# Kernel optimization log

Measured on AMD Instinct MI355X. Metric: run time of the kernel, lower is better.

## Reference

```python
import jax, jax.numpy as jnp
import numpy as np

MODEL_DIM = 1024
H = 16
DK = MODEL_DIM // H


def setup_inputs() -> dict:
    key = jax.random.key(0)
    ks = jax.random.split(key, 11)
    B, S, D = 4, 2048, MODEL_DIM
    s = 1.0 / np.sqrt(D)
    inp = {
        "q": jax.random.normal(ks[0], (B, S, D), jnp.float32),
        "k": jax.random.normal(ks[1], (B, S, D), jnp.float32),
        "v": jax.random.normal(ks[2], (B, S, D), jnp.float32),
        # stacked per-head projection weights [H, D, DK] and biases [H, DK]
        "wq_w": jax.random.normal(ks[3], (H, D, DK), jnp.float32) * s,
        "wq_b": jax.random.normal(ks[4], (H, DK), jnp.float32) * s,
        "wk_w": jax.random.normal(ks[5], (H, D, DK), jnp.float32) * s,
        "wk_b": jax.random.normal(ks[6], (H, DK), jnp.float32) * s,
        "wv_w": jax.random.normal(ks[7], (H, D, DK), jnp.float32) * s,
        "wv_b": jax.random.normal(ks[8], (H, DK), jnp.float32) * s,
        "wo_w": jax.random.normal(ks[9], (D, D), jnp.float32) * s,
        "wo_b": jax.random.normal(ks[10], (D,), jnp.float32) * s,
    }
    return inp


def reference(q, k, v, wq_w, wq_b, wk_w, wk_b, wv_w, wv_b, wo_w, wo_b):
    # per-head projections, batched over heads: [B,S,D] x [H,D,DK] -> [B,H,S,DK]
    qh = jnp.einsum('bsd,hdk->bhsk', q, wq_w) + wq_b[None, :, None, :]
    kh = jnp.einsum('bsd,hdk->bhsk', k, wk_w) + wk_b[None, :, None, :]
    vh = jnp.einsum('bsd,hdk->bhsk', v, wv_w) + wv_b[None, :, None, :]
    scale = 1.0 / jnp.sqrt(jnp.asarray(DK, qh.dtype))
    scores = jnp.einsum('bhqk,bhsk->bhqs', qh, kh) * scale  # [B,H,S,S]
    out = jnp.einsum('bhqs,bhsk->bhqk', scores, vh)         # [B,H,S,DK]
    # NON-STANDARD: softmax applied AFTER the value matmul, over last dim (dv)
    out = jax.nn.softmax(out, axis=-1)
    # concat heads along feature dim: [B,S,H*DK]
    B, Hh, S, Dk = out.shape
    heads = jnp.transpose(out, (0, 2, 1, 3)).reshape(B, S, Hh * Dk)
    return heads @ wo_w.T + wo_b
```

## Files before the change

kernel.cpp:

```cpp
#include <hip/hip_runtime.h>
#include <math.h>

#define B 4
#define S 2048
#define D 1024
#define H 16
#define DK 64
#define MS (B * S)
#define GKA 2048

typedef short bf16x8 __attribute__((ext_vector_type(8)));
typedef float f32x4 __attribute__((ext_vector_type(4)));

__device__ __forceinline__ unsigned short f2bf(float x) {
  union { float f; unsigned u; } v; v.f = x;
  unsigned r = v.u + 0x7fff + ((v.u >> 16) & 1);
  return (unsigned short)(r >> 16);
}
__device__ __forceinline__ float bf2f(unsigned short h) {
  union { unsigned u; float f; } v; v.u = ((unsigned)h) << 16;
  return v.f;
}
__device__ __forceinline__ void split2(float x, unsigned short& hi, unsigned short& lo) {
  hi = f2bf(x);
  lo = f2bf(x - bf2f(hi));
}

__global__ __launch_bounds__(256) void split_a_kernel(
    const float* __restrict__ X0, const float* __restrict__ X1,
    unsigned short* __restrict__ O0, unsigned short* __restrict__ O1) {
  const float* X = blockIdx.z ? X1 : X0;
  unsigned short* O = blockIdx.z ? O1 : O0;
  int t = blockIdx.x * 256 + threadIdx.x;
  int idx = t * 4;
  int m = idx >> 10, d = idx & 1023;
  float4 x = *(const float4*)&X[idx];
  union { unsigned short h[4]; ushort4 u; } uh, ul;
  split2(x.x, uh.h[0], ul.h[0]);
  split2(x.y, uh.h[1], ul.h[1]);
  split2(x.z, uh.h[2], ul.h[2]);
  split2(x.w, uh.h[3], ul.h[3]);
  *(ushort4*)&O[(size_t)m * GKA + d] = uh.u;
  *(ushort4*)&O[(size_t)m * GKA + 1024 + d] = ul.u;
}

__global__ __launch_bounds__(256) void split_wp_kernel(
    const float* __restrict__ W0, const float* __restrict__ W1, const float* __restrict__ W2,
    unsigned short* __restrict__ O0, unsigned short* __restrict__ O1,
    unsigned short* __restrict__ O2) {
  const float* W = blockIdx.z == 0 ? W0 : (blockIdx.z == 1 ? W1 : W2);
  unsigned short* O = blockIdx.z == 0 ? O0 : (blockIdx.z == 1 ? O1 : O2);
  int t = blockIdx.x * 256 + threadIdx.x;
  int d = t & 1023, n = t >> 10;
  int h = n >> 6, dk = n & 63;
  float x = W[((size_t)(h << 10) + d) * 64 + dk];
  unsigned short hi, lo;
  split2(x, hi, lo);
  size_t ro = (size_t)n * GKA + d;
  O[ro] = hi;
  O[ro + 1024] = lo;
}

__global__ __launch_bounds__(256) void wo_cast_kernel(const float* __restrict__ W,
                                                      unsigned short* __restrict__ O) {
  int t = blockIdx.x * 256 + threadIdx.x;
  int idx = t * 4;
  float4 x = *(const float4*)&W[idx];
  ushort4 u;
  u.x = f2bf(x.x); u.y = f2bf(x.y); u.z = f2bf(x.z); u.w = f2bf(x.w);
  *(ushort4*)&O[idx] = u;
}

#define BK 32
template <int SPLIT>
__global__ __launch_bounds__(256) void gemm_kernel(
    const unsigned short* __restrict__ A0, const unsigned short* __restrict__ A1,
    const unsigned short* __restrict__ B0, const unsigned short* __restrict__ B1,
    const float* __restrict__ bias0, const float* __restrict__ bias1,
    float* __restrict__ C0, float* __restrict__ C1) {
  const int KLOG = SPLIT ? 3072 : 1024;
  const int AST = SPLIT ? 2048 : 1024;
  const int BST = SPLIT ? 2048 : 1024;
  const unsigned short* A = blockIdx.z ? A1 : A0;
  const unsigned short* BT = blockIdx.z ? B1 : B0;
  const float* bias = blockIdx.z ? bias1 : bias0;
  float* C = blockIdx.z ? C1 : C0;

  __shared__ __align__(16) unsigned short As[128 * BK];
  __shared__ __align__(16) unsigned short Bs[128 * BK];
  const int tid = threadIdx.x;
  const int lane = tid & 63;
  const int w = tid >> 6;
  const int wm = (w >> 1) * 64;
  const int wn = (w & 1) * 64;
  const size_t bm = (size_t)blockIdx.y * 128;
  const size_t bn = (size_t)blockIdx.x * 128;

  f32x4 acc[4][4];
#pragma unroll
  for (int i = 0; i < 4; i++)
#pragma unroll
    for (int j = 0; j < 4; j++) acc[i][j] = (f32x4){0.f, 0.f, 0.f, 0.f};

  const int srow = lane >> 2;
  const int skof = (lane & 3) * 8;
  const unsigned short* Ag0 = A + (bm + w * 32 + srow) * AST + skof;
  const unsigned short* Ag1 = Ag0 + (size_t)16 * AST;
  const unsigned short* Bg0 = BT + (bn + w * 32 + srow) * BST + skof;
  const unsigned short* Bg1 = Bg0 + (size_t)16 * BST;
  unsigned short* As0 = As + (w * 2) * 512;
  unsigned short* As1 = As0 + 512;
  unsigned short* Bs0 = Bs + (w * 2) * 512;
  unsigned short* Bs1 = Bs0 + 512;

  const int fm = lane & 15;
  const int fk = (lane >> 4) * 8;

  for (int k0 = 0; k0 < KLOG; k0 += BK) {
    const int aofs = SPLIT ? (k0 < 2048 ? k0 : k0 - 2048) : k0;
    const int bofs = SPLIT ? (k0 < 1024 ? k0 : k0 - 1024) : k0;
    __syncthreads();
    __builtin_amdgcn_global_load_lds((const __attribute__((address_space(1))) void*)(Ag0 + aofs),
                                     (__attribute__((address_space(3))) void*)As0, 16, 0, 0);
    __builtin_amdgcn_global_load_lds((const __attribute__((address_space(1))) void*)(Ag1 + aofs),
                                     (__attribute__((address_space(3))) void*)As1, 16, 0, 0);
    __builtin_amdgcn_global_load_lds((const __attribute__((address_space(1))) void*)(Bg0 + bofs),
                                     (__attribute__((address_space(3))) void*)Bs0, 16, 0, 0);
    __builtin_amdgcn_global_load_lds((const __attribute__((address_space(1))) void*)(Bg1 + bofs),
                                     (__attribute__((address_space(3))) void*)Bs1, 16, 0, 0);
    __syncthreads();
    bf16x8 af[4], bf[4];
#pragma unroll
    for (int i = 0; i < 4; i++) {
      af[i] = *(const bf16x8*)&As[(wm + i * 16 + fm) * BK + fk];
      bf[i] = *(const bf16x8*)&Bs[(wn + i * 16 + fm) * BK + fk];
    }
#pragma unroll
    for (int i = 0; i < 4; i++)
#pragma unroll
      for (int j = 0; j < 4; j++)
        acc[i][j] = __builtin_amdgcn_mfma_f32_16x16x32_bf16(af[i], bf[j], acc[i][j], 0, 0, 0);
  }

  const int r0 = (lane >> 4) * 4;
#pragma unroll
  for (int i = 0; i < 4; i++)
#pragma unroll
    for (int j = 0; j < 4; j++) {
      size_t row = bm + wm + i * 16 + r0;
      size_t col = bn + wn + j * 16 + fm;
      float bb = bias[col];
#pragma unroll
      for (int r = 0; r < 4; r++) C[(row + r) * D + col] = acc[i][j][r] + bb;
    }
}

__global__ __launch_bounds__(256) void compute_m_kernel(
    const float* __restrict__ KH, const float* __restrict__ VH, float* __restrict__ Mout) {
  const int sc = blockIdx.x, h = blockIdx.y, b = blockIdx.z;
  const int tid = threadIdx.x;
  const int i0 = (tid >> 4) * 4;
  const int j0 = (tid & 15) * 4;
  __shared__ float ks[16][64], vs[16][64];
  float acc[4][4];
#pragma unroll
  for (int a = 0; a < 4; a++)
#pragma unroll
    for (int c = 0; c < 4; c++) acc[a][c] = 0.f;

  const int s0 = sc * (S / 8);
  const int rr = tid >> 4;
  const int cc = (tid & 15) * 4;
  for (int s = s0; s < s0 + S / 8; s += 16) {
    size_t base = ((size_t)b * S + s + rr) * D + h * 64 + cc;
    __syncthreads();
    *(float4*)&ks[rr][cc] = *(const float4*)&KH[base];
    *(float4*)&vs[rr][cc] = *(const float4*)&VH[base];
    __syncthreads();
#pragma unroll
    for (int ss = 0; ss < 16; ss++) {
      float4 kf = *(const float4*)&ks[ss][i0];
      float4 vf = *(const float4*)&vs[ss][j0];
      float ka[4] = {kf.x, kf.y, kf.z, kf.w};
      float va[4] = {vf.x, vf.y, vf.z, vf.w};
#pragma unroll
      for (int a = 0; a < 4; a++)
#pragma unroll
        for (int c = 0; c < 4; c++) acc[a][c] += ka[a] * va[c];
    }
  }
  float* Mp = Mout + ((size_t)(b * H + h)) * DK * DK;
#pragma unroll
  for (int a = 0; a < 4; a++)
#pragma unroll
    for (int c = 0; c < 4; c++) atomicAdd(&Mp[(i0 + a) * DK + j0 + c], acc[a][c]);
}

__global__ __launch_bounds__(256) void split_m_kernel(const float* __restrict__ M,
                                                      unsigned short* __restrict__ MSP) {
  const int bh = blockIdx.x;
  const float* Mp = M + (size_t)bh * 4096;
  unsigned short* hiP = MSP + (size_t)bh * 8192;
  unsigned short* loP = hiP + 4096;
  for (int idx = threadIdx.x; idx < 4096; idx += 256) {
    int kk = idx >> 6, nn = idx & 63;
    unsigned short hi, lo;
    split2(Mp[idx], hi, lo);
    hiP[nn * 64 + kk] = hi;
    loP[nn * 64 + kk] = lo;
  }
}

__global__ __launch_bounds__(256) void qm_mfma_softmax_kernel(
    const float* __restrict__ QH, const unsigned short* __restrict__ MSP,
    unsigned short* __restrict__ HB) {
  const int sc = blockIdx.x, h = blockIdx.y, b = blockIdx.z;
  const int tid = threadIdx.x;
  const int lane = tid & 63;
  const int w = tid >> 6;

  const int fm = lane & 15;
  const int quad = lane >> 4;
  const int ko = quad * 8;

  const size_t rbase = (size_t)b * S + sc * 64 + w * 16;
  const float* qrow = QH + (rbase + fm) * D + h * 64;
  float qf[16];
  *(float4*)&qf[0] = *(const float4*)&qrow[ko];
  *(float4*)&qf[4] = *(const float4*)&qrow[ko + 4];
  *(float4*)&qf[8] = *(const float4*)&qrow[32 + ko];
  *(float4*)&qf[12] = *(const float4*)&qrow[32 + ko + 4];
  bf16x8 ahi0, alo0, ahi1, alo1;
#pragma unroll
  for (int j = 0; j < 8; j++) {
    unsigned short hi, lo;
    split2(qf[j], hi, lo);
    ahi0[j] = (short)hi; alo0[j] = (short)lo;
    split2(qf[8 + j], hi, lo);
    ahi1[j] = (short)hi; alo1[j] = (short)lo;
  }

  const unsigned short* hiP = MSP + ((size_t)(b * H + h)) * 8192;
  const unsigned short* loP = hiP + 4096;
  bf16x8 bhi[2][4], blo[2][4];
#pragma unroll
  for (int t = 0; t < 2; t++)
#pragma unroll
    for (int j = 0; j < 4; j++) {
      bhi[t][j] = *(const bf16x8*)&hiP[(j * 16 + fm) * 64 + t * 32 + ko];
      blo[t][j] = *(const bf16x8*)&loP[(j * 16 + fm) * 64 + t * 32 + ko];
    }

  f32x4 acc[4];
#pragma unroll
  for (int j = 0; j < 4; j++) acc[j] = (f32x4){0.f, 0.f, 0.f, 0.f};
#pragma unroll
  for (int j = 0; j < 4; j++) {
    acc[j] = __builtin_amdgcn_mfma_f32_16x16x32_bf16(ahi0, bhi[0][j], acc[j], 0, 0, 0);
    acc[j] = __builtin_amdgcn_mfma_f32_16x16x32_bf16(ahi1, bhi[1][j], acc[j], 0, 0, 0);
    acc[j] = __builtin_amdgcn_mfma_f32_16x16x32_bf16(alo0, bhi[0][j], acc[j], 0, 0, 0);
    acc[j] = __builtin_amdgcn_mfma_f32_16x16x32_bf16(alo1, bhi[1][j], acc[j], 0, 0, 0);
    acc[j] = __builtin_amdgcn_mfma_f32_16x16x32_bf16(ahi0, blo[0][j], acc[j], 0, 0, 0);
    acc[j] = __builtin_amdgcn_mfma_f32_16x16x32_bf16(ahi1, blo[1][j], acc[j], 0, 0, 0);
  }

  f32x4 l[4];
#pragma unroll
  for (int j = 0; j < 4; j++)
#pragma unroll
    for (int r = 0; r < 4; r++) l[j][r] = acc[j][r] * 0.125f;

  f32x4 mx = l[0];
#pragma unroll
  for (int j = 1; j < 4; j++)
#pragma unroll
    for (int r = 0; r < 4; r++) mx[r] = fmaxf(mx[r], l[j][r]);
#pragma unroll
  for (int off = 1; off < 16; off <<= 1)
#pragma unroll
    for (int r = 0; r < 4; r++) mx[r] = fmaxf(mx[r], __shfl_xor(mx[r], off, 64));

  f32x4 e[4];
  f32x4 sm = (f32x4){0.f, 0.f, 0.f, 0.f};
#pragma unroll
  for (int j = 0; j < 4; j++)
#pragma unroll
    for (int r = 0; r < 4; r++) {
      e[j][r] = __expf(l[j][r] - mx[r]);
      sm[r] += e[j][r];
    }
#pragma unroll
  for (int off = 1; off < 16; off <<= 1)
#pragma unroll
    for (int r = 0; r < 4; r++) sm[r] += __shfl_xor(sm[r], off, 64);

  f32x4 inv;
#pragma unroll
  for (int r = 0; r < 4; r++) inv[r] = 1.0f / sm[r];

#pragma unroll
  for (int j = 0; j < 4; j++)
#pragma unroll
    for (int r = 0; r < 4; r++) {
      float p = e[j][r] * inv[r];
      HB[(rbase + quad * 4 + r) * D + h * 64 + j * 16 + fm] = f2bf(p);
    }
}

extern "C" void kernel_launch(void* const* d_in, const int* in_sizes, int n_in,
                              void* d_out, int out_size, void* d_ws, size_t ws_size,
                              hipStream_t stream) {
  const float* q = (const float*)d_in[0];
  const float* k = (const float*)d_in[1];
  const float* v = (const float*)d_in[2];
  const float* wq_w = (const float*)d_in[3];
  const float* wq_b = (const float*)d_in[4];
  const float* wk_w = (const float*)d_in[5];
  const float* wk_b = (const float*)d_in[6];
  const float* wv_w = (const float*)d_in[7];
  const float* wv_b = (const float*)d_in[8];
  const float* wo_w = (const float*)d_in[9];
  const float* wo_b = (const float*)d_in[10];
  float* out = (float*)d_out;

  const size_t nProj = (size_t)MS * D;
  float* KH = (float*)d_ws;
  float* VH = KH + nProj;
  float* M = VH + nProj;
  unsigned short* MSP = (unsigned short*)(M + 256 * 1024);
  unsigned short* KSP = MSP + 512 * 1024;
  unsigned short* VSP = KSP + (size_t)16 * 1024 * 1024;
  unsigned short* WQS = VSP + (size_t)16 * 1024 * 1024;
  unsigned short* WKS = WQS + (size_t)2 * 1024 * 1024;
  unsigned short* WVS = WKS + (size_t)2 * 1024 * 1024;
  float* QH = VH;
  QH = (float*)VSP;
  unsigned short* HB = KSP;
  unsigned short* WOB = KSP + (size_t)8 * 1024 * 1024;

  dim3 blk(256);

  hipMemsetAsync(M, 0, (size_t)B * H * DK * DK * sizeof(float), stream);
  split_wp_kernel<<<dim3(4096, 1, 3), blk, 0, stream>>>(wq_w, wk_w, wv_w, WQS, WKS, WVS);
  split_a_kernel<<<dim3(8192, 1, 2), blk, 0, stream>>>(k, v, KSP, VSP);
  gemm_kernel<1><<<dim3(8, 64, 2), blk, 0, stream>>>(KSP, VSP, WKS, WVS, wk_b, wv_b, KH, VH);
  compute_m_kernel<<<dim3(8, H, B), blk, 0, stream>>>(KH, VH, M);
  split_m_kernel<<<64, blk, 0, stream>>>(M, MSP);
  split_a_kernel<<<dim3(8192, 1, 1), blk, 0, stream>>>(q, q, KSP, KSP);
  gemm_kernel<1><<<dim3(8, 64, 1), blk, 0, stream>>>(KSP, KSP, WQS, WQS, wq_b, wq_b, QH, QH);
  wo_cast_kernel<<<1024, blk, 0, stream>>>(wo_w, WOB);
  qm_mfma_softmax_kernel<<<dim3(S / 64, H, B), blk, 0, stream>>>(QH, MSP, HB);
  gemm_kernel<0><<<dim3(8, 64, 1), blk, 0, stream>>>(HB, HB, WOB, WOB, wo_b, wo_b, out, out);
}
```

Measured before the change: 503.7 us.

## Fold K^T V into Q projection weights and fuse softmax into Q GEMM

Instead of projecting Q to fp32 and then multiplying by the per-head M = K^T V, the change precomputes per-batch weights Wq·M (and bias bq·M) and runs a single split-bf16 GEMM from Q whose epilogue applies the scaled softmax and writes bf16 heads. It also merges all input splitting, weight casting and the M zeroing into one prep kernel, and reuses the output buffer for KH. This removes the QH fp32 round trip and a separate small-K attention kernel, but the Q GEMM now reads a per-batch B matrix (4x weight traffic) and the precomputed weights add a small extra kernel.

```diff
diff --git a/kernel.cpp b/kernel.cpp
--- a/kernel.cpp
+++ b/kernel.cpp
@@ -26,49 +26,67 @@
   lo = f2bf(x - bf2f(hi));
 }
 
-__global__ __launch_bounds__(256) void split_a_kernel(
-    const float* __restrict__ X0, const float* __restrict__ X1,
-    unsigned short* __restrict__ O0, unsigned short* __restrict__ O1) {
-  const float* X = blockIdx.z ? X1 : X0;
-  unsigned short* O = blockIdx.z ? O1 : O0;
-  int t = blockIdx.x * 256 + threadIdx.x;
-  int idx = t * 4;
-  int m = idx >> 10, d = idx & 1023;
-  float4 x = *(const float4*)&X[idx];
-  union { unsigned short h[4]; ushort4 u; } uh, ul;
-  split2(x.x, uh.h[0], ul.h[0]);
-  split2(x.y, uh.h[1], ul.h[1]);
-  split2(x.z, uh.h[2], ul.h[2]);
-  split2(x.w, uh.h[3], ul.h[3]);
-  *(ushort4*)&O[(size_t)m * GKA + d] = uh.u;
-  *(ushort4*)&O[(size_t)m * GKA + 1024 + d] = ul.u;
-}
-
-__global__ __launch_bounds__(256) void split_wp_kernel(
-    const float* __restrict__ W0, const float* __restrict__ W1, const float* __restrict__ W2,
-    unsigned short* __restrict__ O0, unsigned short* __restrict__ O1,
-    unsigned short* __restrict__ O2) {
-  const float* W = blockIdx.z == 0 ? W0 : (blockIdx.z == 1 ? W1 : W2);
-  unsigned short* O = blockIdx.z == 0 ? O0 : (blockIdx.z == 1 ? O1 : O2);
-  int t = blockIdx.x * 256 + threadIdx.x;
-  int d = t & 1023, n = t >> 10;
-  int h = n >> 6, dk = n & 63;
-  float x = W[((size_t)(h << 10) + d) * 64 + dk];
-  unsigned short hi, lo;
-  split2(x, hi, lo);
-  size_t ro = (size_t)n * GKA + d;
-  O[ro] = hi;
-  O[ro + 1024] = lo;
-}
-
-__global__ __launch_bounds__(256) void wo_cast_kernel(const float* __restrict__ W,
-                                                      unsigned short* __restrict__ O) {
-  int t = blockIdx.x * 256 + threadIdx.x;
-  int idx = t * 4;
-  float4 x = *(const float4*)&W[idx];
-  ushort4 u;
-  u.x = f2bf(x.x); u.y = f2bf(x.y); u.z = f2bf(x.z); u.w = f2bf(x.w);
-  *(ushort4*)&O[idx] = u;
+__global__ __launch_bounds__(256) void prep_kernel(
+    const float* __restrict__ q, const float* __restrict__ k, const float* __restrict__ v,
+    const float* __restrict__ wk, const float* __restrict__ wv, const float* __restrict__ wq,
+    const float* __restrict__ wo,
+    unsigned short* __restrict__ KSP, unsigned short* __restrict__ VSP,
+    unsigned short* __restrict__ QSP,
+    unsigned short* __restrict__ WKS, unsigned short* __restrict__ WVS,
+    unsigned short* __restrict__ WQA, unsigned short* __restrict__ WOB,
+    float* __restrict__ M) {
+  const int blk = blockIdx.x;
+  const int tid = threadIdx.x;
+  if (blk < 24576) {
+    const int which = blk >> 13;
+    const int bb = blk & 8191;
+    const float* X = which == 0 ? k : (which == 1 ? v : q);
+    unsigned short* O = which == 0 ? KSP : (which == 1 ? VSP : QSP);
+    int t = bb * 256 + tid;
+    int idx = t * 4;
+    int m = idx >> 10, d = idx & 1023;
+    float4 x = *(const float4*)&X[idx];
+    union { unsigned short h[4]; ushort4 u; } uh, ul;
+    split2(x.x, uh.h[0], ul.h[0]);
+    split2(x.y, uh.h[1], ul.h[1]);
+    split2(x.z, uh.h[2], ul.h[2]);
+    split2(x.w, uh.h[3], ul.h[3]);
+    *(ushort4*)&O[(size_t)m * GKA + d] = uh.u;
+    *(ushort4*)&O[(size_t)m * GKA + 1024 + d] = ul.u;
+  } else if (blk < 32768) {
+    const int which = (blk - 24576) >> 12;
+    const int bb = (blk - 24576) & 4095;
+    const float* W = which == 0 ? wk : wv;
+    unsigned short* O = which == 0 ? WKS : WVS;
+    int t = bb * 256 + tid;
+    int d = t & 1023, n = t >> 10;
+    int h = n >> 6, dk = n & 63;
+    float x = W[((size_t)(h << 10) + d) * 64 + dk];
+    unsigned short hi, lo;
+    split2(x, hi, lo);
+    size_t ro = (size_t)n * GKA + d;
+    O[ro] = hi;
+    O[ro + 1024] = lo;
+  } else if (blk < 36864) {
+    int t = (blk - 32768) * 256 + tid;
+    int kk = t & 63;
+    int hd = t >> 6;
+    float x = wq[t];
+    unsigned short hi, lo;
+    split2(x, hi, lo);
+    WQA[(size_t)hd * 128 + kk] = hi;
+    WQA[(size_t)hd * 128 + 64 + kk] = lo;
+  } else if (blk < 37888) {
+    int t = (blk - 36864) * 256 + tid;
+    int idx = t * 4;
+    float4 x = *(const float4*)&wo[idx];
+    ushort4 u;
+    u.x = f2bf(x.x); u.y = f2bf(x.y); u.z = f2bf(x.z); u.w = f2bf(x.w);
+    *(ushort4*)&WOB[idx] = u;
+  } else {
+    int t = (blk - 37888) * 256 + tid;
+    *(float4*)&M[(size_t)t * 4] = (float4){0.f, 0.f, 0.f, 0.f};
+  }
 }
 
 #define BK 32
@@ -155,6 +173,120 @@
     }
 }
 
+__global__ __launch_bounds__(256) void gemm_q_softmax(
+    const unsigned short* __restrict__ A, const unsigned short* __restrict__ WQM,
+    const float* __restrict__ BQM, unsigned short* __restrict__ HB) {
+  const int b = blockIdx.y >> 4;
+  const unsigned short* BT = WQM + (size_t)b * D * GKA;
+
+  __shared__ __align__(16) unsigned short As[128 * BK];
+  __shared__ __align__(16) unsigned short Bs[128 * BK];
+  const int tid = threadIdx.x;
+  const int lane = tid & 63;
+  const int w = tid >> 6;
+  const int wm = (w >> 1) * 64;
+  const int wn = (w & 1) * 64;
+  const size_t bm = (size_t)blockIdx.y * 128;
+  const size_t bn = (size_t)blockIdx.x * 128;
+
+  f32x4 acc[4][4];
+#pragma unroll
+  for (int i = 0; i < 4; i++)
+#pragma unroll
+    for (int j = 0; j < 4; j++) acc[i][j] = (f32x4){0.f, 0.f, 0.f, 0.f};
+
+  const int srow = lane >> 2;
+  const int skof = (lane & 3) * 8;
+  const unsigned short* Ag0 = A + (bm + w * 32 + srow) * GKA + skof;
+  const unsigned short* Ag1 = Ag0 + (size_t)16 * GKA;
+  const unsigned short* Bg0 = BT + (bn + w * 32 + srow) * GKA + skof;
+  const unsigned short* Bg1 = Bg0 + (size_t)16 * GKA;
+  unsigned short* As0 = As + (w * 2) * 512;
+  unsigned short* As1 = As0 + 512;
+  unsigned short* Bs0 = Bs + (w * 2) * 512;
+  unsigned short* Bs1 = Bs0 + 512;
+
+  const int fm = lane & 15;
+  const int fk = (lane >> 4) * 8;
+
+  for (int k0 = 0; k0 < 3072; k0 += BK) {
+    const int aofs = (k0 < 2048) ? k0 : k0 - 2048;
+    const int bofs = (k0 < 1024) ? k0 : k0 - 1024;
+    __syncthreads();
+    __builtin_amdgcn_global_load_lds((const __attribute__((address_space(1))) void*)(Ag0 + aofs),
+                                     (__attribute__((address_space(3))) void*)As0, 16, 0, 0);
+    __builtin_amdgcn_global_load_lds((const __attribute__((address_space(1))) void*)(Ag1 + aofs),
+                                     (__attribute__((address_space(3))) void*)As1, 16, 0, 0);
+    __builtin_amdgcn_global_load_lds((const __attribute__((address_space(1))) void*)(Bg0 + bofs),
+                                     (__attribute__((address_space(3))) void*)Bs0, 16, 0, 0);
+    __builtin_amdgcn_global_load_lds((const __attribute__((address_space(1))) void*)(Bg1 + bofs),
+                                     (__attribute__((address_space(3))) void*)Bs1, 16, 0, 0);
+    __syncthreads();
+    bf16x8 af[4], bf[4];
+#pragma unroll
+    for (int i = 0; i < 4; i++) {
+      af[i] = *(const bf16x8*)&As[(wm + i * 16 + fm) * BK + fk];
+      bf[i] = *(const bf16x8*)&Bs[(wn + i * 16 + fm) * BK + fk];
+    }
+#pragma unroll
+    for (int i = 0; i < 4; i++)
+#pragma unroll
+      for (int j = 0; j < 4; j++)
+        acc[i][j] = __builtin_amdgcn_mfma_f32_16x16x32_bf16(af[i], bf[j], acc[i][j], 0, 0, 0);
+  }
+
+  const int quad = lane >> 4;
+  const size_t head_col0 = bn + wn;
+  float bj[4];
+#pragma unroll
+  for (int j = 0; j < 4; j++) bj[j] = BQM[(size_t)b * D + head_col0 + j * 16 + fm];
+
+#pragma unroll
+  for (int i = 0; i < 4; i++) {
+    f32x4 val[4];
+#pragma unroll
+    for (int j = 0; j < 4; j++)
+#pragma unroll
+      for (int r = 0; r < 4; r++) val[j][r] = (acc[i][j][r] + bj[j]) * 0.125f;
+
+    f32x4 mx = val[0];
+#pragma unroll
+    for (int j = 1; j < 4; j++)
+#pragma unroll
+      for (int r = 0; r < 4; r++) mx[r] = fmaxf(mx[r], val[j][r]);
+#pragma unroll
+    for (int off = 1; off < 16; off <<= 1)
+#pragma unroll
+      for (int r = 0; r < 4; r++) mx[r] = fmaxf(mx[r], __shfl_xor(mx[r], off, 64));
+
+    f32x4 e[4];
+    f32x4 sm = (f32x4){0.f, 0.f, 0.f, 0.f};
+#pragma unroll
+    for (int j = 0; j < 4; j++)
+#pragma unroll
+      for (int r = 0; r < 4; r++) {
+        e[j][r] = __expf(val[j][r] - mx[r]);
+        sm[r] += e[j][r];
+      }
+#pragma unroll
+    for (int off = 1; off < 16; off <<= 1)
+#pragma unroll
+      for (int r = 0; r < 4; r++) sm[r] += __shfl_xor(sm[r], off, 64);
+
+    f32x4 inv;
+#pragma unroll
+    for (int r = 0; r < 4; r++) inv[r] = 1.0f / sm[r];
+
+#pragma unroll
+    for (int j = 0; j < 4; j++)
+#pragma unroll
+      for (int r = 0; r < 4; r++) {
+        size_t row = bm + wm + i * 16 + quad * 4 + r;
+        HB[row * D + head_col0 + j * 16 + fm] = f2bf(e[j][r] * inv[r]);
+      }
+  }
+}
+
 __global__ __launch_bounds__(256) void compute_m_kernel(
     const float* __restrict__ KH, const float* __restrict__ VH, float* __restrict__ Mout) {
   const int sc = blockIdx.x, h = blockIdx.y, b = blockIdx.z;
@@ -196,9 +328,11 @@
     for (int c = 0; c < 4; c++) atomicAdd(&Mp[(i0 + a) * DK + j0 + c], acc[a][c]);
 }
 
-__global__ __launch_bounds__(256) void split_m_kernel(const float* __restrict__ M,
-                                                      unsigned short* __restrict__ MSP) {
+__global__ __launch_bounds__(256) void split_m_bias_kernel(
+    const float* __restrict__ M, const float* __restrict__ bq,
+    unsigned short* __restrict__ MSP, float* __restrict__ BQM) {
   const int bh = blockIdx.x;
+  const int h = bh & 15;
   const float* Mp = M + (size_t)bh * 4096;
   unsigned short* hiP = MSP + (size_t)bh * 8192;
   unsigned short* loP = hiP + 4096;
@@ -209,102 +343,65 @@
     hiP[nn * 64 + kk] = hi;
     loP[nn * 64 + kk] = lo;
   }
-}
-
-__global__ __launch_bounds__(256) void qm_mfma_softmax_kernel(
-    const float* __restrict__ QH, const unsigned short* __restrict__ MSP,
-    unsigned short* __restrict__ HB) {
-  const int sc = blockIdx.x, h = blockIdx.y, b = blockIdx.z;
+  if (threadIdx.x < 64) {
+    int j = threadIdx.x;
+    float a = 0.f;
+#pragma unroll 8
+    for (int kk = 0; kk < 64; kk++) a += bq[h * 64 + kk] * Mp[kk * 64 + j];
+    BQM[(size_t)bh * 64 + j] = a;
+  }
+}
+
+__global__ __launch_bounds__(256) void wqm_kernel(
+    const unsigned short* __restrict__ WQA, const unsigned short* __restrict__ MSP,
+    unsigned short* __restrict__ WQM) {
+  const int c = blockIdx.x, h = blockIdx.y, b = blockIdx.z;
   const int tid = threadIdx.x;
   const int lane = tid & 63;
   const int w = tid >> 6;
-
   const int fm = lane & 15;
   const int quad = lane >> 4;
   const int ko = quad * 8;
-
-  const size_t rbase = (size_t)b * S + sc * 64 + w * 16;
-  const float* qrow = QH + (rbase + fm) * D + h * 64;
-  float qf[16];
-  *(float4*)&qf[0] = *(const float4*)&qrow[ko];
-  *(float4*)&qf[4] = *(const float4*)&qrow[ko + 4];
-  *(float4*)&qf[8] = *(const float4*)&qrow[32 + ko];
-  *(float4*)&qf[12] = *(const float4*)&qrow[32 + ko + 4];
-  bf16x8 ahi0, alo0, ahi1, alo1;
-#pragma unroll
-  for (int j = 0; j < 8; j++) {
-    unsigned short hi, lo;
-    split2(qf[j], hi, lo);
-    ahi0[j] = (short)hi; alo0[j] = (short)lo;
-    split2(qf[8 + j], hi, lo);
-    ahi1[j] = (short)hi; alo1[j] = (short)lo;
-  }
+  const int dbase = c * 64 + w * 16;
+
+  const unsigned short* arow = WQA + ((size_t)h * 1024 + dbase + fm) * 128;
+  bf16x8 ahi0 = *(const bf16x8*)&arow[ko];
+  bf16x8 ahi1 = *(const bf16x8*)&arow[32 + ko];
+  bf16x8 alo0 = *(const bf16x8*)&arow[64 + ko];
+  bf16x8 alo1 = *(const bf16x8*)&arow[96 + ko];
 
   const unsigned short* hiP = MSP + ((size_t)(b * H + h)) * 8192;
   const unsigned short* loP = hiP + 4096;
-  bf16x8 bhi[2][4], blo[2][4];
-#pragma unroll
-  for (int t = 0; t < 2; t++)
-#pragma unroll
-    for (int j = 0; j < 4; j++) {
-      bhi[t][j] = *(const bf16x8*)&hiP[(j * 16 + fm) * 64 + t * 32 + ko];
-      blo[t][j] = *(const bf16x8*)&loP[(j * 16 + fm) * 64 + t * 32 + ko];
-    }
-
   f32x4 acc[4];
 #pragma unroll
   for (int j = 0; j < 4; j++) acc[j] = (f32x4){0.f, 0.f, 0.f, 0.f};
 #pragma unroll
   for (int j = 0; j < 4; j++) {
-    acc[j] = __builtin_amdgcn_mfma_f32_16x16x32_bf16(ahi0, bhi[0][j], acc[j], 0, 0, 0);
-    acc[j] = __builtin_amdgcn_mfma_f32_16x16x32_bf16(ahi1, bhi[1][j], acc[j], 0, 0, 0);
-    acc[j] = __builtin_amdgcn_mfma_f32_16x16x32_bf16(alo0, bhi[0][j], acc[j], 0, 0, 0);
-    acc[j] = __builtin_amdgcn_mfma_f32_16x16x32_bf16(alo1, bhi[1][j], acc[j], 0, 0, 0);
-    acc[j] = __builtin_amdgcn_mfma_f32_16x16x32_bf16(ahi0, blo[0][j], acc[j], 0, 0, 0);
-    acc[j] = __builtin_amdgcn_mfma_f32_16x16x32_bf16(ahi1, blo[1][j], acc[j], 0, 0, 0);
-  }
-
-  f32x4 l[4];
-#pragma unroll
-  for (int j = 0; j < 4; j++)
-#pragma unroll
-    for (int r = 0; r < 4; r++) l[j][r] = acc[j][r] * 0.125f;
-
-  f32x4 mx = l[0];
-#pragma unroll
-  for (int j = 1; j < 4; j++)
-#pragma unroll
-    for (int r = 0; r < 4; r++) mx[r] = fmaxf(mx[r], l[j][r]);
-#pragma unroll
-  for (int off = 1; off < 16; off <<= 1)
-#pragma unroll
-    for (int r = 0; r < 4; r++) mx[r] = fmaxf(mx[r], __shfl_xor(mx[r], off, 64));
-
-  f32x4 e[4];
-  f32x4 sm = (f32x4){0.f, 0.f, 0.f, 0.f};
-#pragma unroll
-  for (int j = 0; j < 4; j++)
-#pragma unroll
-    for (int r = 0; r < 4; r++) {
-      e[j][r] = __expf(l[j][r] - mx[r]);
-      sm[r] += e[j][r];
-    }
-#pragma unroll
-  for (int off = 1; off < 16; off <<= 1)
-#pragma unroll
-    for (int r = 0; r < 4; r++) sm[r] += __shfl_xor(sm[r], off, 64);
-
-  f32x4 inv;
-#pragma unroll
-  for (int r = 0; r < 4; r++) inv[r] = 1.0f / sm[r];
-
-#pragma unroll
-  for (int j = 0; j < 4; j++)
-#pragma unroll
-    for (int r = 0; r < 4; r++) {
-      float p = e[j][r] * inv[r];
-      HB[(rbase + quad * 4 + r) * D + h * 64 + j * 16 + fm] = f2bf(p);
-    }
+    bf16x8 bhi0 = *(const bf16x8*)&hiP[(j * 16 + fm) * 64 + ko];
+    bf16x8 bhi1 = *(const bf16x8*)&hiP[(j * 16 + fm) * 64 + 32 + ko];
+    bf16x8 blo0 = *(const bf16x8*)&loP[(j * 16 + fm) * 64 + ko];
+    bf16x8 blo1 = *(const bf16x8*)&loP[(j * 16 + fm) * 64 + 32 + ko];
+    acc[j] = __builtin_amdgcn_mfma_f32_16x16x32_bf16(ahi0, bhi0, acc[j], 0, 0, 0);
+    acc[j] = __builtin_amdgcn_mfma_f32_16x16x32_bf16(ahi1, bhi1, acc[j], 0, 0, 0);
+    acc[j] = __builtin_amdgcn_mfma_f32_16x16x32_bf16(alo0, bhi0, acc[j], 0, 0, 0);
+    acc[j] = __builtin_amdgcn_mfma_f32_16x16x32_bf16(alo1, bhi1, acc[j], 0, 0, 0);
+    acc[j] = __builtin_amdgcn_mfma_f32_16x16x32_bf16(ahi0, blo0, acc[j], 0, 0, 0);
+    acc[j] = __builtin_amdgcn_mfma_f32_16x16x32_bf16(ahi1, blo1, acc[j], 0, 0, 0);
+  }
+
+#pragma unroll
+  for (int j = 0; j < 4; j++) {
+    int n = h * 64 + j * 16 + fm;
+    ushort4 hv, lv;
+    unsigned short hi, lo;
+    split2(acc[j][0], hi, lo); hv.x = hi; lv.x = lo;
+    split2(acc[j][1], hi, lo); hv.y = hi; lv.y = lo;
+    split2(acc[j][2], hi, lo); hv.z = hi; lv.z = lo;
+    split2(acc[j][3], hi, lo); hv.w = hi; lv.w = lo;
+    size_t base = ((size_t)b * D + n) * GKA + dbase + quad * 4;
+    *(ushort4*)&WQM[base] = hv;
+    *(ushort4*)&WQM[base + 1024] = lv;
+  }
 }
 
 extern "C" void kernel_launch(void* const* d_in, const int* in_sizes, int n_in,
@@ -323,32 +420,29 @@
   const float* wo_b = (const float*)d_in[10];
   float* out = (float*)d_out;
 
-  const size_t nProj = (size_t)MS * D;
-  float* KH = (float*)d_ws;
-  float* VH = KH + nProj;
-  float* M = VH + nProj;
-  unsigned short* MSP = (unsigned short*)(M + 256 * 1024);
-  unsigned short* KSP = MSP + 512 * 1024;
+  unsigned short* KSP = (unsigned short*)d_ws;
   unsigned short* VSP = KSP + (size_t)16 * 1024 * 1024;
-  unsigned short* WQS = VSP + (size_t)16 * 1024 * 1024;
-  unsigned short* WKS = WQS + (size_t)2 * 1024 * 1024;
+  unsigned short* QSP = VSP + (size_t)16 * 1024 * 1024;
+  float* VH = (float*)(QSP + (size_t)16 * 1024 * 1024);
+  float* M = VH + (size_t)MS * D;
+  unsigned short* WKS = (unsigned short*)(M + 256 * 1024);
   unsigned short* WVS = WKS + (size_t)2 * 1024 * 1024;
-  float* QH = VH;
-  QH = (float*)VSP;
+  unsigned short* WQA = WVS + (size_t)2 * 1024 * 1024;
+  unsigned short* WOB = WQA + (size_t)2 * 1024 * 1024;
+  float* KH = out;
   unsigned short* HB = KSP;
-  unsigned short* WOB = KSP + (size_t)8 * 1024 * 1024;
+  unsigned short* WQM = KSP + (size_t)8 * 1024 * 1024;
+  unsigned short* MSP = VSP;
+  float* BQM = (float*)(VSP + 512 * 1024);
 
   dim3 blk(256);
 
-  hipMemsetAsync(M, 0, (size_t)B * H * DK * DK * sizeof(float), stream);
-  split_wp_kernel<<<dim3(4096, 1, 3), blk, 0, stream>>>(wq_w, wk_w, wv_w, WQS, WKS, WVS);
-  split_a_kernel<<<dim3(8192, 1, 2), blk, 0, stream>>>(k, v, KSP, VSP);
+  prep_kernel<<<38144, blk, 0, stream>>>(q, k, v, wk_w, wv_w, wq_w, wo_w,
+                                         KSP, VSP, QSP, WKS, WVS, WQA, WOB, M);
   gemm_kernel<1><<<dim3(8, 64, 2), blk, 0, stream>>>(KSP, VSP, WKS, WVS, wk_b, wv_b, KH, VH);
   compute_m_kernel<<<dim3(8, H, B), blk, 0, stream>>>(KH, VH, M);
-  split_m_kernel<<<64, blk, 0, stream>>>(M, MSP);
-  split_a_kernel<<<dim3(8192, 1, 1), blk, 0, stream>>>(q, q, KSP, KSP);
-  gemm_kernel<1><<<dim3(8, 64, 1), blk, 0, stream>>>(KSP, KSP, WQS, WQS, wq_b, wq_b, QH, QH);
-  wo_cast_kernel<<<1024, blk, 0, stream>>>(wo_w, WOB);
-  qm_mfma_softmax_kernel<<<dim3(S / 64, H, B), blk, 0, stream>>>(QH, MSP, HB);
+  split_m_bias_kernel<<<64, blk, 0, stream>>>(M, wq_b, MSP, BQM);
+  wqm_kernel<<<dim3(16, H, B), blk, 0, stream>>>(WQA, MSP, WQM);
+  gemm_q_softmax<<<dim3(8, 64), blk, 0, stream>>>(QSP, WQM, BQM, HB);
   gemm_kernel<0><<<dim3(8, 64, 1), blk, 0, stream>>>(HB, HB, WOB, WOB, wo_b, wo_b, out, out);
 }
```

After: 480.2 us. -4.7%, faster.
